# Kernel optimization log

Measured on AMD Instinct MI355X. Metric: run time of the kernel, lower is better.

The kernel has to match this reference:

```python
import jax, jax.numpy as jnp
import numpy as np

B, T, E, H = 4, 2048, 1024, 2048  # note: T must equal H (mask shape constraint in source)


def setup_inputs() -> dict:
    key = jax.random.key(0)
    ks = jax.random.split(key, 5)
    x = jax.random.normal(ks[0], (B, T, E), dtype=jnp.float32)
    Wq = jax.random.normal(ks[1], (E, H), dtype=jnp.float32) * 0.02
    bq = jnp.zeros((H,), dtype=jnp.float32)
    Wv = jax.random.normal(ks[2], (E, H), dtype=jnp.float32) * 0.02
    bv = jnp.zeros((H,), dtype=jnp.float32)
    return {"x": x, "Wq": Wq, "bq": bq, "Wv": Wv, "bv": bv}


def reference(x, Wq, bq, Wv, bv):
    # NOTE: original code uses q_proj for BOTH q and k (k = self.q_proj(x)),
    # so k is identical to q; k_proj params are dead. We reproduce that.
    q = x @ Wq + bq                                  # [B, T, H]
    v = x @ Wv + bv                                  # [B, T, H]
    scores = jnp.einsum('bqd,bkd->bqk', q, q)        # q @ k.mT with k == q
    scaled = scores / jnp.sqrt(jnp.float32(Wq.shape[1]))
    mask = jnp.tril(jnp.ones((scaled.shape[1], scaled.shape[2]), dtype=scaled.dtype))
    masked = scaled * mask                           # multiplicative mask (as in source)
    attn = jax.nn.softmax(masked, axis=1)            # softmax over dim=1 (query axis), as in source
    return attn @ v                                  # [B, T, H]
```

## Files before the change

### kernel.cpp

```cpp
#include <hip/hip_runtime.h>


#define B_DIM 4
#define T_DIM 2048
#define E_DIM 1024
#define H_DIM 2048

typedef __attribute__((ext_vector_type(8))) short bf16x8;
typedef __attribute__((ext_vector_type(4))) short s16x4;
typedef __attribute__((ext_vector_type(4))) float f32x4;

__device__ __forceinline__ float bf2f(short s) {
  union { float f; unsigned u; } x; x.u = ((unsigned)(unsigned short)s) << 16; return x.f;
}
__device__ __forceinline__ short f2bf(float f) {
  union { float f; unsigned u; } x; x.f = f;
  unsigned r = x.u + 0x7fff + ((x.u >> 16) & 1);
  return (short)(r >> 16);
}

__device__ __forceinline__ void gload16(const short* g, short* l) {
  __builtin_amdgcn_global_load_lds(
      (const __attribute__((address_space(1))) void*)g,
      (__attribute__((address_space(3))) void*)l, 16, 0, 0);
}

__device__ __forceinline__ void bar() {
  __builtin_amdgcn_sched_barrier(0);
  __builtin_amdgcn_s_barrier();
  __builtin_amdgcn_sched_barrier(0);
}

template<int MODE>
__global__ __launch_bounds__(512, 2) void gemm256(
    const short* __restrict__ Ag, const short* __restrict__ Bg,
    const float* __restrict__ bias, const float* __restrict__ bias2,
    void* __restrict__ Cg, void* __restrict__ Cg2,
    const float* __restrict__ sfx,
    int N, int K, long sA, long sB, long sC)
{
  __shared__ __align__(16) short lds[2 * 32768];

  const int t = threadIdx.x;
  const int lane = t & 63, wave = t >> 6;
  const int wm = wave >> 2, wn = wave & 3;
  const int l16 = lane & 15, kg = lane >> 4;

  int rt, ct, bz;
  if (MODE == 2) { rt = blockIdx.x; ct = blockIdx.y; bz = blockIdx.z; }
  else {
    int lin = blockIdx.y * gridDim.x + blockIdx.x;
    const int cpx = (gridDim.x * gridDim.y) >> 3;
    lin = (lin & 7) * cpx + (lin >> 3);
    rt = lin / gridDim.x; ct = lin - rt * gridDim.x;
    bz = 0;
  }

  const short* A  = Ag + (long)bz * sA + (long)rt * 256 * K;
  const short* Bp = Bg + (long)bz * sB + (long)ct * 256 * K;
  const int kEnd = (MODE == 2) ? (rt + 1) * 256 : K;
  const int NT = kEnd >> 6;

  long soff[2];
  int dsto[2];
#pragma unroll
  for (int j = 0; j < 2; ++j) {
    const int cid = j * 512 + t;
    const int f = cid >> 3, sl = cid & 7;
    const int c = sl ^ (f & 7);
    soff[j] = (long)(2 * f + (c >> 2)) * K + (c & 3) * 8;
    dsto[j] = cid * 8;
  }

  const int fl = l16 >> 1;
  const int slot = (((l16 & 1) * 4 + kg) ^ fl) & 7;
  const int aoff = (wm * 64 + fl) * 64 + slot * 8;
  const int boff = (wn * 32 + fl) * 64 + slot * 8;

  f32x4 acc[8][4] = {};

  {
    short* S = lds;
#pragma unroll
    for (int kh = 0; kh < 2; ++kh)
#pragma unroll
      for (int j = 0; j < 2; ++j) {
        gload16(A  + soff[j] + kh * 32, &S[kh * 8192 + dsto[j]]);
        gload16(Bp + soff[j] + kh * 32, &S[16384 + kh * 8192 + dsto[j]]);
      }
  }
  asm volatile("s_waitcnt vmcnt(4)");
  __builtin_amdgcn_sched_barrier(0);
  bar();

  for (int T = 0; T < NT; ++T) {
    const short* Abase = lds + (T & 1) * 32768;
    short* S = lds + ((T + 1) & 1) * 32768;
    const long kIss = (long)(T + 1) * 64;
    const bool st = (T + 1) < NT;
    bf16x8 bfr[4], af[4];

    {
      const short* Ab = Abase;
      const short* Bb = Abase + 16384;
#pragma unroll
      for (int n = 0; n < 4; ++n) bfr[n] = *(const bf16x8*)&Bb[boff + n * 512];
#pragma unroll
      for (int m = 0; m < 4; ++m) af[m] = *(const bf16x8*)&Ab[aoff + m * 512];
      if (st) {
        gload16(A + soff[0] + kIss, &S[dsto[0]]);
        gload16(A + soff[1] + kIss, &S[dsto[1]]);
      }
      bar();
      __builtin_amdgcn_s_setprio(1);
#pragma unroll
      for (int m = 0; m < 4; ++m)
#pragma unroll
        for (int n = 0; n < 4; ++n)
          acc[m][n] = __builtin_amdgcn_mfma_f32_16x16x32_bf16(af[m], bfr[n], acc[m][n], 0, 0, 0);
      __builtin_amdgcn_s_setprio(0);
      bar();
    }
    {
      const short* Ab = Abase;
#pragma unroll
      for (int m = 0; m < 4; ++m) af[m] = *(const bf16x8*)&Ab[aoff + (m + 4) * 512];
      if (st) {
        gload16(Bp + soff[0] + kIss, &S[16384 + dsto[0]]);
        gload16(Bp + soff[1] + kIss, &S[16384 + dsto[1]]);
      }
      bar();
      __builtin_amdgcn_s_setprio(1);
#pragma unroll
      for (int m = 0; m < 4; ++m)
#pragma unroll
        for (int n = 0; n < 4; ++n)
          acc[m + 4][n] = __builtin_amdgcn_mfma_f32_16x16x32_bf16(af[m], bfr[n], acc[m + 4][n], 0, 0, 0);
      __builtin_amdgcn_s_setprio(0);
      if (T == NT - 1) asm volatile("s_waitcnt vmcnt(0)");
      else             asm volatile("s_waitcnt vmcnt(4)");
      __builtin_amdgcn_sched_barrier(0);
      bar();
    }
    {
      const short* Ab = Abase + 8192;
      const short* Bb = Abase + 16384 + 8192;
#pragma unroll
      for (int n = 0; n < 4; ++n) bfr[n] = *(const bf16x8*)&Bb[boff + n * 512];
#pragma unroll
      for (int m = 0; m < 4; ++m) af[m] = *(const bf16x8*)&Ab[aoff + m * 512];
      if (st) {
        gload16(A + soff[0] + kIss + 32, &S[8192 + dsto[0]]);
        gload16(A + soff[1] + kIss + 32, &S[8192 + dsto[1]]);
      }
      bar();
      __builtin_amdgcn_s_setprio(1);
#pragma unroll
      for (int m = 0; m < 4; ++m)
#pragma unroll
        for (int n = 0; n < 4; ++n)
          acc[m][n] = __builtin_amdgcn_mfma_f32_16x16x32_bf16(af[m], bfr[n], acc[m][n], 0, 0, 0);
      __builtin_amdgcn_s_setprio(0);
      bar();
    }
    {
      const short* Ab = Abase + 8192;
#pragma unroll
      for (int m = 0; m < 4; ++m) af[m] = *(const bf16x8*)&Ab[aoff + (m + 4) * 512];
      if (st) {
        gload16(Bp + soff[0] + kIss + 32, &S[16384 + 8192 + dsto[0]]);
        gload16(Bp + soff[1] + kIss + 32, &S[16384 + 8192 + dsto[1]]);
      }
      bar();
      __builtin_amdgcn_s_setprio(1);
#pragma unroll
      for (int m = 0; m < 4; ++m)
#pragma unroll
        for (int n = 0; n < 4; ++n)
          acc[m + 4][n] = __builtin_amdgcn_mfma_f32_16x16x32_bf16(af[m], bfr[n], acc[m + 4][n], 0, 0, 0);
      __builtin_amdgcn_s_setprio(0);
      if (st) {
        asm volatile("s_waitcnt vmcnt(4)");
        __builtin_amdgcn_sched_barrier(0);
      }
      bar();
    }
  }

  __syncthreads();

  if (MODE == 0) {
    short* Cs = lds;
    const int Nh = N >> 1;
#pragma unroll
    for (int m = 0; m < 8; ++m)
#pragma unroll
      for (int n = 0; n < 4; ++n) {
        const int cl = wn * 64 + n * 16 + l16;
        const int colg = ct * 256 + cl;
        const float bv = (colg < Nh) ? bias[colg] : bias2[colg - Nh];
#pragma unroll
        for (int r = 0; r < 4; ++r) {
          const int rl = wm * 128 + m * 16 + kg * 4 + r;
          *(short*)((char*)Cs + (((((rl << 8) + cl) << 1)) ^ ((rl & 7) << 4))) =
              f2bf(acc[m][n][r] + bv);
        }
      }
    __syncthreads();
    short* C = ((ct * 256) < Nh) ? (short*)Cg : (short*)Cg2;
    const int rr = t >> 1, hc = (t & 1) * 128;
    const long gbase = (long)(rt * 256 + rr) * Nh + ((ct * 256) & (Nh - 1)) + hc;
#pragma unroll
    for (int j = 0; j < 16; ++j)
      *(bf16x8*)(C + gbase + j * 8) =
          *(const bf16x8*)((const char*)Cs +
              ((((rr << 8) + hc + (j << 3)) << 1) ^ ((rr & 7) << 4)));
  } else {
    float* C = (float*)Cg + (long)bz * sC;
    const float* sf = sfx + ((long)bz * 16 + 2 * rt + 1) * N;
    const int rowb = rt * 256 + wm * 128 + kg * 4;
    const int colb = ct * 256 + wn * 64 + l16;
#pragma unroll
    for (int m = 0; m < 8; ++m)
#pragma unroll
      for (int n = 0; n < 4; ++n) {
        const int col = colb + n * 16;
        const float s = sf[col];
#pragma unroll
        for (int r = 0; r < 4; ++r)
          C[(long)(rowb + m * 16 + r) * N + col] = acc[m][n][r] + s;
      }
  }
}

template<int MODE>
__global__ __launch_bounds__(256) void gemm_bt(
    const short* __restrict__ Ag, const short* __restrict__ Bg,
    const float* __restrict__ bias, const float* __restrict__ bias2,
    void* __restrict__ Cg, void* __restrict__ Cg2,
    float* __restrict__ colsum, const float* __restrict__ sfx,
    int M, int N, int K, long sA, long sB, long sC, float scale)
{
  __shared__ __align__(16) short lds[128 * 64 * 2];
  short* As = lds;
  short* Bs = lds + 128 * 64;
  __shared__ float csum[128];

  const int t = threadIdx.x;
  const int bz = blockIdx.z;

  int rt, ct;
  if (MODE == 1) {
    int idx = 135 - blockIdx.x;
    rt = (int)((sqrtf(8.0f * idx + 1.0f) - 1.0f) * 0.5f);
    while ((rt + 1) * (rt + 2) / 2 <= idx) rt++;
    while (rt * (rt + 1) / 2 > idx) rt--;
    ct = idx - rt * (rt + 1) / 2;
  } else {
    rt = blockIdx.y; ct = blockIdx.x;
  }

  const short* A = Ag + (long)bz * sA + (long)rt * 128 * K;
  const short* B = Bg + (long)bz * sB + (long)ct * 128 * K;
  const int kEnd = K;

  const int lane = t & 63;
  const int wave = t >> 6;
  const int wr = wave >> 1, wc = wave & 1;
  const int l16 = lane & 15, kg = lane >> 4;

  if (MODE == 1) { if (t < 128) csum[t] = (rt == ct) ? 128.0f * ct : 0.0f; }

  f32x4 acc[4][4] = {};

  for (int k0 = 0; k0 < kEnd; k0 += 64) {
    __syncthreads();
#pragma unroll
    for (int j = 0; j < 4; ++j) {
      const int e = j * 256 + t;
      const int r = e >> 3, cl = e & 7;
      const int cg = cl ^ (r & 7);
      gload16(A + (long)r * K + (k0 + cg * 8), &As[e * 8]);
      gload16(B + (long)r * K + (k0 + cg * 8), &Bs[e * 8]);
    }
    __syncthreads();
#pragma unroll
    for (int kk = 0; kk < 2; ++kk) {
      bf16x8 af[4], bfr[4];
#pragma unroll
      for (int mi = 0; mi < 4; ++mi)
        af[mi] = *(const bf16x8*)&As[(wr * 64 + mi * 16 + l16) * 64 +
                                     ((kk * 4 + kg) ^ (l16 & 7)) * 8];
#pragma unroll
      for (int ni = 0; ni < 4; ++ni)
        bfr[ni] = *(const bf16x8*)&Bs[(wc * 64 + ni * 16 + l16) * 64 +
                                      ((kk * 4 + kg) ^ (l16 & 7)) * 8];
#pragma unroll
      for (int mi = 0; mi < 4; ++mi)
#pragma unroll
        for (int ni = 0; ni < 4; ++ni)
          acc[mi][ni] = __builtin_amdgcn_mfma_f32_16x16x32_bf16(af[mi], bfr[ni], acc[mi][ni], 0, 0, 0);
    }
  }

  if (MODE == 1) {
    short* Cs = lds;
    __syncthreads();
    float ps[4] = {0.f, 0.f, 0.f, 0.f};
#pragma unroll
    for (int mi = 0; mi < 4; ++mi)
#pragma unroll
      for (int ni = 0; ni < 4; ++ni) {
        const int cl = wc * 64 + ni * 16 + l16;
        const int col = ct * 128 + cl;
#pragma unroll
        for (int r = 0; r < 4; ++r) {
          const int rl = wr * 64 + kg * 4 + mi * 16 + r;
          const int row = rt * 128 + rl;
          float e = (row >= col) ? __expf(acc[mi][ni][r] * scale) : 1.0f;
          Cs[rl * 128 + cl] = f2bf(e);
          ps[ni] += e;
        }
      }
#pragma unroll
    for (int ni = 0; ni < 4; ++ni)
      atomicAdd(&csum[wc * 64 + ni * 16 + l16], ps[ni]);
    __syncthreads();
    short* C = (short*)Cg + (long)bz * sC;
    const int rr = t >> 1, cc = (t & 1) * 64;
    const long gbase = (long)(rt * 128 + rr) * N + ct * 128 + cc;
#pragma unroll
    for (int j = 0; j < 8; ++j)
      *(bf16x8*)(C + gbase + j * 8) = *(const bf16x8*)&Cs[rr * 128 + cc + j * 8];
    if (t < 128)
      atomicAdd(&colsum[(long)bz * N + ct * 128 + t], csum[t]);
  }
}

__global__ __launch_bounds__(256) void ones_fill(short* __restrict__ P)
{
  const int r = blockIdx.x, bz = blockIdx.z;
  short* p = P + (long)bz * T_DIM * T_DIM +
             (long)(2 * r) * 128 * T_DIM + (2 * r + 1) * 128;
  const int t = threadIdx.x;
  const int row = t >> 1, c0 = (t & 1) * 64;
  bf16x8 ones;
#pragma unroll
  for (int j = 0; j < 8; ++j) ones[j] = (short)0x3F80;
#pragma unroll
  for (int j = 0; j < 8; ++j)
    *(bf16x8*)(p + (long)row * T_DIM + c0 + j * 8) = ones;
}

__global__ __launch_bounds__(256) void f32_to_bf16(
    const float* __restrict__ src, short* __restrict__ dst, long n)
{
  long i = ((long)blockIdx.x * blockDim.x + threadIdx.x) * 4;
  if (i < n) {
    const float4 v = *(const float4*)(src + i);
    s16x4 o;
    o.x = f2bf(v.x); o.y = f2bf(v.y); o.z = f2bf(v.z); o.w = f2bf(v.w);
    *(s16x4*)(dst + i) = o;
  }
}

__global__ __launch_bounds__(256) void wtrans(
    const float* __restrict__ src0, const float* __restrict__ src1,
    short* __restrict__ dst)
{
  __shared__ short tile[64][65];
  const int t = threadIdx.x;
  const int c0 = blockIdx.x * 64;
  const int r0 = blockIdx.y * 64;
  const float* s = blockIdx.z ? src1 : src0;
  short* d = dst + (long)blockIdx.z * H_DIM * E_DIM;
  const int rl = t >> 4, cb = (t & 15) * 4;
#pragma unroll
  for (int i = 0; i < 4; ++i) {
    int r = rl + i * 16;
    const float4 w = *(const float4*)(s + (long)(r0 + r) * H_DIM + c0 + cb);
    tile[r][cb + 0] = f2bf(w.x); tile[r][cb + 1] = f2bf(w.y);
    tile[r][cb + 2] = f2bf(w.z); tile[r][cb + 3] = f2bf(w.w);
  }
  __syncthreads();
#pragma unroll
  for (int i = 0; i < 4; ++i) {
    int rr = rl + i * 16;
    s16x4 o;
    o.x = tile[cb + 0][rr]; o.y = tile[cb + 1][rr];
    o.z = tile[cb + 2][rr]; o.w = tile[cb + 3][rr];
    *(s16x4*)(d + (long)(c0 + rr) * E_DIM + r0 + cb) = o;
  }
}

__global__ __launch_bounds__(256) void vtrans(
    const short* __restrict__ src, short* __restrict__ dst,
    const float* __restrict__ sums)
{
  __shared__ short tile[64][65];
  const int t = threadIdx.x;
  const int c0 = blockIdx.x * 64;
  const int r0 = blockIdx.y * 64;
  const int bz = blockIdx.z;
  const short* s = src + (long)bz * T_DIM * H_DIM;
  short* d = dst + (long)bz * H_DIM * T_DIM;
  const float* su = sums + (long)bz * T_DIM;
  const int rl = t >> 4, cb = (t & 15) * 4;
#pragma unroll
  for (int i = 0; i < 4; ++i) {
    int r = rl + i * 16;
    const float rs = 1.0f / su[r0 + r];
    const s16x4 w = *(const s16x4*)(s + (long)(r0 + r) * H_DIM + c0 + cb);
    tile[r][cb + 0] = f2bf(bf2f(w.x) * rs); tile[r][cb + 1] = f2bf(bf2f(w.y) * rs);
    tile[r][cb + 2] = f2bf(bf2f(w.z) * rs); tile[r][cb + 3] = f2bf(bf2f(w.w) * rs);
  }
  __syncthreads();
#pragma unroll
  for (int i = 0; i < 4; ++i) {
    int rr = rl + i * 16;
    s16x4 o;
    o.x = tile[cb + 0][rr]; o.y = tile[cb + 1][rr];
    o.z = tile[cb + 2][rr]; o.w = tile[cb + 3][rr];
    *(s16x4*)(d + (long)(c0 + rr) * T_DIM + r0 + cb) = o;
  }
}

__global__ __launch_bounds__(256) void block_psum(
    const short* __restrict__ v, const float* __restrict__ colsum,
    float* __restrict__ psum)
{
  const int h = (blockIdx.x * 256 + threadIdx.x) * 2;
  const int j = blockIdx.y, bz = blockIdx.z;
  const short* vb = v + (long)bz * T_DIM * H_DIM;
  const float* cs = colsum + (long)bz * T_DIM;
  float s0 = 0.f, s1 = 0.f;
  const int k0 = j * 128;
  for (int k = k0; k < k0 + 128; ++k) {
    union { int i; short s[2]; } w;
    w.i = *(const int*)(vb + (long)k * H_DIM + h);
    const float rs = 1.0f / cs[k];
    s0 += bf2f(w.s[0]) * rs;
    s1 += bf2f(w.s[1]) * rs;
  }
  float* p = psum + ((long)bz * 16 + j) * H_DIM + h;
  p[0] = s0; p[1] = s1;
}

__global__ __launch_bounds__(256) void suffix_scan(
    const float* __restrict__ psum, float* __restrict__ sfx)
{
  const int h = blockIdx.x * 256 + threadIdx.x;
  const int bz = blockIdx.z;
  const long base = (long)bz * 16 * H_DIM + h;
  float suf = 0.f;
  sfx[base + 15L * H_DIM] = 0.f;
  for (int j = 15; j >= 1; --j) {
    suf += psum[base + (long)j * H_DIM];
    sfx[base + (long)(j - 1) * H_DIM] = suf;
  }
}

extern "C" void kernel_launch(void* const* d_in, const int* in_sizes, int n_in,
                              void* d_out, int out_size, void* d_ws, size_t ws_size,
                              hipStream_t stream) {
  const float* x  = (const float*)d_in[0];
  const float* Wq = (const float*)d_in[1];
  const float* bq = (const float*)d_in[2];
  const float* Wv = (const float*)d_in[3];
  const float* bv = (const float*)d_in[4];
  float* out = (float*)d_out;

  char* ws = (char*)d_ws;
  short* P      = (short*)(ws);
  short* q      = (short*)(ws + (size_t)32 * 1024 * 1024);
  short* v      = (short*)(ws + (size_t)64 * 1024 * 1024);
  float* colsum = (float*)(ws + (size_t)96 * 1024 * 1024);
  float* sfx    = (float*)(ws + (size_t)96 * 1024 * 1024 + 32 * 1024);
  short* vT = q;

  short* xb    = (short*)d_out;
  short* WqvT  = (short*)((char*)d_out + (size_t)16 * 1024 * 1024);
  float* psum  = (float*)((char*)d_out + (size_t)24 * 1024 * 1024);

  const float scale = 0.022097086912079612f;
  dim3 blk(256);

  hipMemsetAsync(colsum, 0, (size_t)B_DIM * T_DIM * 4, stream);

  f32_to_bf16<<<dim3((B_DIM * T_DIM * E_DIM) / (256 * 4)), blk, 0, stream>>>(
      x, xb, (long)B_DIM * T_DIM * E_DIM);
  wtrans<<<dim3(H_DIM / 64, E_DIM / 64, 2), blk, 0, stream>>>(Wq, Wv, WqvT);

  gemm256<0><<<dim3((2 * H_DIM) / 256, (B_DIM * T_DIM) / 256, 1), dim3(512), 0, stream>>>(
      xb, WqvT, bq, bv, q, v, nullptr, 2 * H_DIM, E_DIM, 0, 0, 0);

  gemm_bt<1><<<dim3(136, 1, B_DIM), blk, 0, stream>>>(
      q, q, nullptr, nullptr, P, nullptr, colsum, nullptr, T_DIM, T_DIM, H_DIM,
      (long)T_DIM * H_DIM, (long)T_DIM * H_DIM, (long)T_DIM * T_DIM, scale);

  ones_fill<<<dim3(8, 1, B_DIM), blk, 0, stream>>>(P);

  vtrans<<<dim3(H_DIM / 64, T_DIM / 64, B_DIM), blk, 0, stream>>>(v, vT, colsum);
  block_psum<<<dim3(H_DIM / 512, 16, B_DIM), blk, 0, stream>>>(v, colsum, psum);
  suffix_scan<<<dim3(H_DIM / 256, 1, B_DIM), blk, 0, stream>>>(psum, sfx);

  gemm256<2><<<dim3(T_DIM / 256, H_DIM / 256, B_DIM), dim3(512), 0, stream>>>(
      P, vT, nullptr, nullptr, out, nullptr, sfx, H_DIM, T_DIM,
      (long)T_DIM * T_DIM, (long)H_DIM * T_DIM, (long)T_DIM * H_DIM);
}
```

Baseline: 352.6 us.

## Simplify GEMM main loop to one barrier per K-tile with bulk prefetch

```diff
diff --git a/kernel.cpp b/kernel.cpp
--- a/kernel.cpp
+++ b/kernel.cpp
@@ -23,12 +23,6 @@
   __builtin_amdgcn_global_load_lds(
       (const __attribute__((address_space(1))) void*)g,
       (__attribute__((address_space(3))) void*)l, 16, 0, 0);
-}
-
-__device__ __forceinline__ void bar() {
-  __builtin_amdgcn_sched_barrier(0);
-  __builtin_amdgcn_s_barrier();
-  __builtin_amdgcn_sched_barrier(0);
 }
 
 template<int MODE>
@@ -89,101 +83,58 @@
         gload16(Bp + soff[j] + kh * 32, &S[16384 + kh * 8192 + dsto[j]]);
       }
   }
-  asm volatile("s_waitcnt vmcnt(4)");
+  asm volatile("s_waitcnt vmcnt(0)");
   __builtin_amdgcn_sched_barrier(0);
-  bar();
+  __builtin_amdgcn_s_barrier();
+  __builtin_amdgcn_sched_barrier(0);
 
   for (int T = 0; T < NT; ++T) {
-    const short* Abase = lds + (T & 1) * 32768;
+    const short* Ab = lds + (T & 1) * 32768;
     short* S = lds + ((T + 1) & 1) * 32768;
-    const long kIss = (long)(T + 1) * 64;
     const bool st = (T + 1) < NT;
-    bf16x8 bfr[4], af[4];
-
-    {
-      const short* Ab = Abase;
-      const short* Bb = Abase + 16384;
-#pragma unroll
-      for (int n = 0; n < 4; ++n) bfr[n] = *(const bf16x8*)&Bb[boff + n * 512];
-#pragma unroll
-      for (int m = 0; m < 4; ++m) af[m] = *(const bf16x8*)&Ab[aoff + m * 512];
-      if (st) {
-        gload16(A + soff[0] + kIss, &S[dsto[0]]);
-        gload16(A + soff[1] + kIss, &S[dsto[1]]);
-      }
-      bar();
-      __builtin_amdgcn_s_setprio(1);
-#pragma unroll
-      for (int m = 0; m < 4; ++m)
-#pragma unroll
-        for (int n = 0; n < 4; ++n)
-          acc[m][n] = __builtin_amdgcn_mfma_f32_16x16x32_bf16(af[m], bfr[n], acc[m][n], 0, 0, 0);
-      __builtin_amdgcn_s_setprio(0);
-      bar();
+
+    if (st) {
+      const long kI = (long)(T + 1) * 64;
+      gload16(A  + soff[0] + kI, &S[dsto[0]]);
+      gload16(A  + soff[1] + kI, &S[dsto[1]]);
+      gload16(Bp + soff[0] + kI, &S[16384 + dsto[0]]);
+      gload16(Bp + soff[1] + kI, &S[16384 + dsto[1]]);
+      gload16(A  + soff[0] + kI + 32, &S[8192 + dsto[0]]);
+      gload16(A  + soff[1] + kI + 32, &S[8192 + dsto[1]]);
+      gload16(Bp + soff[0] + kI + 32, &S[16384 + 8192 + dsto[0]]);
+      gload16(Bp + soff[1] + kI + 32, &S[16384 + 8192 + dsto[1]]);
     }
-    {
-      const short* Ab = Abase;
-#pragma unroll
-      for (int m = 0; m < 4; ++m) af[m] = *(const bf16x8*)&Ab[aoff + (m + 4) * 512];
-      if (st) {
-        gload16(Bp + soff[0] + kIss, &S[16384 + dsto[0]]);
-        gload16(Bp + soff[1] + kIss, &S[16384 + dsto[1]]);
-      }
-      bar();
-      __builtin_amdgcn_s_setprio(1);
-#pragma unroll
-      for (int m = 0; m < 4; ++m)
-#pragma unroll
-        for (int n = 0; n < 4; ++n)
-          acc[m + 4][n] = __builtin_amdgcn_mfma_f32_16x16x32_bf16(af[m], bfr[n], acc[m + 4][n], 0, 0, 0);
-      __builtin_amdgcn_s_setprio(0);
-      if (T == NT - 1) asm volatile("s_waitcnt vmcnt(0)");
-      else             asm volatile("s_waitcnt vmcnt(4)");
+    __builtin_amdgcn_sched_barrier(0);
+
+    bf16x8 af[8], bfr[4];
+#pragma unroll
+    for (int n = 0; n < 4; ++n) bfr[n] = *(const bf16x8*)&Ab[16384 + boff + n * 512];
+#pragma unroll
+    for (int m = 0; m < 8; ++m) af[m] = *(const bf16x8*)&Ab[aoff + m * 512];
+    __builtin_amdgcn_s_setprio(1);
+#pragma unroll
+    for (int m = 0; m < 8; ++m)
+#pragma unroll
+      for (int n = 0; n < 4; ++n)
+        acc[m][n] = __builtin_amdgcn_mfma_f32_16x16x32_bf16(af[m], bfr[n], acc[m][n], 0, 0, 0);
+    __builtin_amdgcn_s_setprio(0);
+#pragma unroll
+    for (int n = 0; n < 4; ++n) bfr[n] = *(const bf16x8*)&Ab[16384 + 8192 + boff + n * 512];
+#pragma unroll
+    for (int m = 0; m < 8; ++m) af[m] = *(const bf16x8*)&Ab[8192 + aoff + m * 512];
+    __builtin_amdgcn_s_setprio(1);
+#pragma unroll
+    for (int m = 0; m < 8; ++m)
+#pragma unroll
+      for (int n = 0; n < 4; ++n)
+        acc[m][n] = __builtin_amdgcn_mfma_f32_16x16x32_bf16(af[m], bfr[n], acc[m][n], 0, 0, 0);
+    __builtin_amdgcn_s_setprio(0);
+
+    if (st) {
+      asm volatile("s_waitcnt vmcnt(0)");
       __builtin_amdgcn_sched_barrier(0);
-      bar();
-    }
-    {
-      const short* Ab = Abase + 8192;
-      const short* Bb = Abase + 16384 + 8192;
-#pragma unroll
-      for (int n = 0; n < 4; ++n) bfr[n] = *(const bf16x8*)&Bb[boff + n * 512];
-#pragma unroll
-      for (int m = 0; m < 4; ++m) af[m] = *(const bf16x8*)&Ab[aoff + m * 512];
-      if (st) {
-        gload16(A + soff[0] + kIss + 32, &S[8192 + dsto[0]]);
-        gload16(A + soff[1] + kIss + 32, &S[8192 + dsto[1]]);
-      }
-      bar();
-      __builtin_amdgcn_s_setprio(1);
-#pragma unroll
-      for (int m = 0; m < 4; ++m)
-#pragma unroll
-        for (int n = 0; n < 4; ++n)
-          acc[m][n] = __builtin_amdgcn_mfma_f32_16x16x32_bf16(af[m], bfr[n], acc[m][n], 0, 0, 0);
-      __builtin_amdgcn_s_setprio(0);
-      bar();
-    }
-    {
-      const short* Ab = Abase + 8192;
-#pragma unroll
-      for (int m = 0; m < 4; ++m) af[m] = *(const bf16x8*)&Ab[aoff + (m + 4) * 512];
-      if (st) {
-        gload16(Bp + soff[0] + kIss + 32, &S[16384 + 8192 + dsto[0]]);
-        gload16(Bp + soff[1] + kIss + 32, &S[16384 + 8192 + dsto[1]]);
-      }
-      bar();
-      __builtin_amdgcn_s_setprio(1);
-#pragma unroll
-      for (int m = 0; m < 4; ++m)
-#pragma unroll
-        for (int n = 0; n < 4; ++n)
-          acc[m + 4][n] = __builtin_amdgcn_mfma_f32_16x16x32_bf16(af[m], bfr[n], acc[m + 4][n], 0, 0, 0);
-      __builtin_amdgcn_s_setprio(0);
-      if (st) {
-        asm volatile("s_waitcnt vmcnt(4)");
-        __builtin_amdgcn_sched_barrier(0);
-      }
-      bar();
+      __builtin_amdgcn_s_barrier();
+      __builtin_amdgcn_sched_barrier(0);
     }
   }
 
```

Measured after the change: 353.2 us. Within noise of the previous version (+0.2%).

## Replace 256-row causal P@V GEMM with 128-row tile kernel and drop ones_fill

Applied to the files above, without the earlier changes.

```diff
diff --git a/kernel.cpp b/kernel.cpp
--- a/kernel.cpp
+++ b/kernel.cpp
@@ -29,6 +29,88 @@
   __builtin_amdgcn_sched_barrier(0);
   __builtin_amdgcn_s_barrier();
   __builtin_amdgcn_sched_barrier(0);
+}
+
+__global__ __launch_bounds__(512, 2) void gemm_pv(
+    const short* __restrict__ Pg, const short* __restrict__ Vg,
+    float* __restrict__ Cg, const float* __restrict__ sfx)
+{
+  __shared__ __align__(16) short lds[24576];
+
+  const int t = threadIdx.x;
+  const int lane = t & 63, wave = t >> 6;
+  const int wm = wave >> 2, wn = wave & 3;
+  const int l16 = lane & 15, kg = lane >> 4;
+
+  const int lin = blockIdx.x + 256 * blockIdx.y;
+  const int rt = 15 - (lin >> 5);
+  const int rem = lin & 31;
+  const int ct = rem >> 2, bz = rem & 3;
+
+  const int K = T_DIM, N = H_DIM;
+  const short* A  = Pg + (long)bz * T_DIM * T_DIM + (long)rt * 128 * K;
+  const short* Bv = Vg + (long)bz * H_DIM * T_DIM + (long)ct * 256 * K;
+  const int NT = (rt + 1) * 2;
+
+  const int fA = t >> 3, cA = (t & 7) ^ (fA & 7);
+  const long sA0 = (long)(2 * fA + (cA >> 2)) * K + (cA & 3) * 8;
+  const int dA0 = t * 8;
+  long sB[2]; int dB[2];
+#pragma unroll
+  for (int j = 0; j < 2; ++j) {
+    const int cid = j * 512 + t;
+    const int f = cid >> 3, c = (cid & 7) ^ (f & 7);
+    sB[j] = (long)(2 * f + (c >> 2)) * K + (c & 3) * 8;
+    dB[j] = cid * 8;
+  }
+
+  const int fl = l16 >> 1;
+  const int slot = (((l16 & 1) * 4 + kg) ^ fl) & 7;
+  const int abase = (wm * 32 + fl) * 64 + slot * 8;
+  const int bbase = 8192 + (wn * 32 + fl) * 64 + slot * 8;
+
+  f32x4 acc[4][4] = {};
+
+  for (int tt = 0; tt < NT; ++tt) {
+    const long k0 = (long)tt * 64;
+    __syncthreads();
+    gload16(A  + sA0   + k0,      &lds[dA0]);
+    gload16(A  + sA0   + k0 + 32, &lds[4096 + dA0]);
+    gload16(Bv + sB[0] + k0,      &lds[8192 + dB[0]]);
+    gload16(Bv + sB[1] + k0,      &lds[8192 + dB[1]]);
+    gload16(Bv + sB[0] + k0 + 32, &lds[16384 + dB[0]]);
+    gload16(Bv + sB[1] + k0 + 32, &lds[16384 + dB[1]]);
+    __syncthreads();
+#pragma unroll
+    for (int kk = 0; kk < 2; ++kk) {
+      bf16x8 bfr[4];
+#pragma unroll
+      for (int ni = 0; ni < 4; ++ni)
+        bfr[ni] = *(const bf16x8*)&lds[bbase + kk * 8192 + ni * 512];
+#pragma unroll
+      for (int mi = 0; mi < 4; ++mi) {
+        const bf16x8 a = *(const bf16x8*)&lds[abase + kk * 4096 + mi * 512];
+#pragma unroll
+        for (int ni = 0; ni < 4; ++ni)
+          acc[mi][ni] = __builtin_amdgcn_mfma_f32_16x16x32_bf16(a, bfr[ni], acc[mi][ni], 0, 0, 0);
+      }
+    }
+  }
+
+  float* C = Cg + (long)bz * T_DIM * H_DIM;
+  const float* sf = sfx + ((long)bz * 16 + rt) * N;
+  const int rowb = rt * 128 + wm * 64 + kg * 4;
+  const int colb = ct * 256 + wn * 64 + l16;
+#pragma unroll
+  for (int mi = 0; mi < 4; ++mi)
+#pragma unroll
+    for (int ni = 0; ni < 4; ++ni) {
+      const int col = colb + ni * 16;
+      const float s = sf[col];
+#pragma unroll
+      for (int r = 0; r < 4; ++r)
+        C[(long)(rowb + mi * 16 + r) * N + col] = acc[mi][ni][r] + s;
+    }
 }
 
 template<int MODE>
@@ -47,8 +129,7 @@
   const int l16 = lane & 15, kg = lane >> 4;
 
   int rt, ct, bz;
-  if (MODE == 2) { rt = blockIdx.x; ct = blockIdx.y; bz = blockIdx.z; }
-  else {
+  {
     int lin = blockIdx.y * gridDim.x + blockIdx.x;
     const int cpx = (gridDim.x * gridDim.y) >> 3;
     lin = (lin & 7) * cpx + (lin >> 3);
@@ -58,7 +139,7 @@
 
   const short* A  = Ag + (long)bz * sA + (long)rt * 256 * K;
   const short* Bp = Bg + (long)bz * sB + (long)ct * 256 * K;
-  const int kEnd = (MODE == 2) ? (rt + 1) * 256 : K;
+  const int kEnd = K;
   const int NT = kEnd >> 6;
 
   long soff[2];
@@ -189,7 +270,7 @@
 
   __syncthreads();
 
-  if (MODE == 0) {
+  {
     short* Cs = lds;
     const int Nh = N >> 1;
 #pragma unroll
@@ -215,21 +296,6 @@
       *(bf16x8*)(C + gbase + j * 8) =
           *(const bf16x8*)((const char*)Cs +
               ((((rr << 8) + hc + (j << 3)) << 1) ^ ((rr & 7) << 4)));
-  } else {
-    float* C = (float*)Cg + (long)bz * sC;
-    const float* sf = sfx + ((long)bz * 16 + 2 * rt + 1) * N;
-    const int rowb = rt * 256 + wm * 128 + kg * 4;
-    const int colb = ct * 256 + wn * 64 + l16;
-#pragma unroll
-    for (int m = 0; m < 8; ++m)
-#pragma unroll
-      for (int n = 0; n < 4; ++n) {
-        const int col = colb + n * 16;
-        const float s = sf[col];
-#pragma unroll
-        for (int r = 0; r < 4; ++r)
-          C[(long)(rowb + m * 16 + r) * N + col] = acc[m][n][r] + s;
-      }
   }
 }
 
@@ -250,14 +316,12 @@
   const int bz = blockIdx.z;
 
   int rt, ct;
-  if (MODE == 1) {
+  {
     int idx = 135 - blockIdx.x;
     rt = (int)((sqrtf(8.0f * idx + 1.0f) - 1.0f) * 0.5f);
     while ((rt + 1) * (rt + 2) / 2 <= idx) rt++;
     while (rt * (rt + 1) / 2 > idx) rt--;
     ct = idx - rt * (rt + 1) / 2;
-  } else {
-    rt = blockIdx.y; ct = blockIdx.x;
   }
 
   const short* A = Ag + (long)bz * sA + (long)rt * 128 * K;
@@ -269,7 +333,7 @@
   const int wr = wave >> 1, wc = wave & 1;
   const int l16 = lane & 15, kg = lane >> 4;
 
-  if (MODE == 1) { if (t < 128) csum[t] = (rt == ct) ? 128.0f * ct : 0.0f; }
+  if (t < 128) csum[t] = (rt == ct) ? 128.0f * ct : 0.0f;
 
   f32x4 acc[4][4] = {};
 
@@ -303,7 +367,7 @@
     }
   }
 
-  if (MODE == 1) {
+  {
     short* Cs = lds;
     __syncthreads();
     float ps[4] = {0.f, 0.f, 0.f, 0.f};
@@ -335,21 +399,6 @@
     if (t < 128)
       atomicAdd(&colsum[(long)bz * N + ct * 128 + t], csum[t]);
   }
-}
-
-__global__ __launch_bounds__(256) void ones_fill(short* __restrict__ P)
-{
-  const int r = blockIdx.x, bz = blockIdx.z;
-  short* p = P + (long)bz * T_DIM * T_DIM +
-             (long)(2 * r) * 128 * T_DIM + (2 * r + 1) * 128;
-  const int t = threadIdx.x;
-  const int row = t >> 1, c0 = (t & 1) * 64;
-  bf16x8 ones;
-#pragma unroll
-  for (int j = 0; j < 8; ++j) ones[j] = (short)0x3F80;
-#pragma unroll
-  for (int j = 0; j < 8; ++j)
-    *(bf16x8*)(p + (long)row * T_DIM + c0 + j * 8) = ones;
 }
 
 __global__ __launch_bounds__(256) void f32_to_bf16(
@@ -498,13 +547,9 @@
       q, q, nullptr, nullptr, P, nullptr, colsum, nullptr, T_DIM, T_DIM, H_DIM,
       (long)T_DIM * H_DIM, (long)T_DIM * H_DIM, (long)T_DIM * T_DIM, scale);
 
-  ones_fill<<<dim3(8, 1, B_DIM), blk, 0, stream>>>(P);
-
   vtrans<<<dim3(H_DIM / 64, T_DIM / 64, B_DIM), blk, 0, stream>>>(v, vT, colsum);
   block_psum<<<dim3(H_DIM / 512, 16, B_DIM), blk, 0, stream>>>(v, colsum, psum);
   suffix_scan<<<dim3(H_DIM / 256, 1, B_DIM), blk, 0, stream>>>(psum, sfx);
 
-  gemm256<2><<<dim3(T_DIM / 256, H_DIM / 256, B_DIM), dim3(512), 0, stream>>>(
-      P, vT, nullptr, nullptr, out, nullptr, sfx, H_DIM, T_DIM,
-      (long)T_DIM * T_DIM, (long)H_DIM * T_DIM, (long)T_DIM * H_DIM);
-}
+  gemm_pv<<<dim3(256, 2, 1), dim3(512), 0, stream>>>(P, vT, out, sfx);
+}
```

Measured after the change: 343.1 us. -2.7%, faster.
